# Kernel tuning notes

Hardware: AMD Instinct MI355X
Metric: run time of the kernel (lower is better)

The kernel has to match this reference:

```python
import jax, jax.numpy as jnp
import numpy as np

K_MASK = -2.3819763e+38
B, T, D = 2, 2048, 2048
N, K, H = 8, 2, 256          # query heads, kv heads, head dim
F = 8192                     # ffn hidden
A = 4                        # num_altup_inputs
P = 4                        # num_modalities
WINDOW = 512
SOFT_CAP = 50.0
Q_SCALE = H ** -0.5
ROPE_BASE = 10000.0


def rms_norm(x, scale=None, eps=1e-6):
    y = x * jax.lax.rsqrt(jnp.mean(jnp.square(x), axis=-1, keepdims=True) + eps)
    if scale is not None:
        y = y * (1.0 + scale)   # scale_plus_one=True
    return y


def apply_rope(x, pos, base=ROPE_BASE, scale_factor=1.0):
    # x: [B,T,num_heads,H], pos: [B,T]
    h = x.shape[-1]
    frac = 2.0 * jnp.arange(h // 2, dtype=jnp.float32) / h
    timescale = base ** frac
    sin_inp = (pos[..., None].astype(jnp.float32) / timescale)[..., None, :] / scale_factor  # [B,T,1,H/2]
    sin, cos = jnp.sin(sin_inp), jnp.cos(sin_inp)
    x1, x2 = jnp.split(x, 2, axis=-1)
    return jnp.concatenate([x1 * cos - x2 * sin, x2 * cos + x1 * sin], axis=-1).astype(x.dtype)


def setup_inputs():
    key = jax.random.key(0)
    ks = jax.random.split(key, 12)
    r = lambda i, shape, s=0.02: jax.random.normal(ks[i], shape, dtype=jnp.float32) * s
    pos = jnp.broadcast_to(jnp.arange(T, dtype=jnp.int32), (B, T))
    causal = pos[:, :, None] >= pos[:, None, :]  # [B,T,T] bool
    return dict(
        x=jax.random.normal(ks[0], (A, B, T, D), dtype=jnp.float32),
        segment_pos=pos,
        attn_mask=causal,
        router_w=r(1, (D, P), 1.0),
        pred_coefs=r(2, (P, A, A), 0.0001),
        corr_coefs=r(3, (P, A), 0.01),
        correct_output_scale=jnp.ones((D,), jnp.float32),
        pre_attn_scale=jnp.zeros((D,), jnp.float32),
        q_w=r(4, (N, D, H)),
        kv_w=r(5, (2, K, D, H)),
        qk_q_scale=jnp.zeros((H,), jnp.float32),
        qk_k_scale=jnp.zeros((H,), jnp.float32),
        o_w=r(6, (N, H, D)),
        post_attn_scale=jnp.zeros((D,), jnp.float32),
        pre_ffw_scale=jnp.zeros((D,), jnp.float32),
        gate_w=r(7, (D, F)),
        up_w=r(8, (D, F)),
        down_w=r(9, (F, D)),
        post_ffw_scale=jnp.zeros((D,), jnp.float32),
    )


def _router(h, router_w):
    # modality router: scale by 1/d_model, project, tanh in fp32
    return jnp.tanh(jnp.einsum('btd,dp->btp', h * (1.0 / D), router_w).astype(jnp.float32))


def _attention(x, segment_pos, attn_mask, q_w, kv_w, qk_q_scale, qk_k_scale, o_w):
    q = jnp.einsum('btd,ndh->btnh', x, q_w)               # [B,T,N,H]
    k, v = jnp.einsum('bsd,ckdh->cbskh', x, kv_w)         # each [B,T,K,H]
    q = rms_norm(q, qk_q_scale)                           # qk norm
    k = rms_norm(k, qk_k_scale)
    v = rms_norm(v)                                       # value norm (no scale)
    q = apply_rope(q, segment_pos) * Q_SCALE
    k = apply_rope(k, segment_pos)
    g = N // K                                            # GQA group size
    qr = q.reshape(B, T, K, g, H)
    logits = jnp.einsum('btkgh,bskh->btkgs', qr, k).reshape(B, T, N, T)
    logits = jnp.tanh(logits / SOFT_CAP) * SOFT_CAP       # attn_logits_soft_cap
    # sliding-window mask combined with causal attn_mask
    sliding = (segment_pos[:, None, :] > segment_pos[:, :, None] - WINDOW) & \
              (segment_pos[:, None, :] < segment_pos[:, :, None] + WINDOW)
    mask = attn_mask & sliding
    padded = jnp.where(mask[:, :, None, :], logits, K_MASK)
    probs = jax.nn.softmax(padded, axis=-1).astype(k.dtype)
    enc = jnp.einsum('btkgs,bskh->btkgh', probs.reshape(B, T, K, g, T), v).reshape(B, T, N, H)
    return jnp.einsum('btnh,nhd->btd', enc, o_w)


def reference(x, segment_pos, attn_mask, router_w, pred_coefs, corr_coefs,
              correct_output_scale, pre_attn_scale, q_w, kv_w, qk_q_scale, qk_k_scale,
              o_w, post_attn_scale, pre_ffw_scale, gate_w, up_w, down_w, post_ffw_scale):
    # ---- AltUp predict ----
    mods = _router(x[0], router_w)                                   # [B,T,P]
    coefs = jnp.einsum('btp,pij->btij', mods, pred_coefs.astype(jnp.float32))
    predictions = x + jnp.einsum('btij,jbtd->ibtd', coefs, x).astype(x.dtype)
    active = predictions[0]
    # ---- attention block ----
    attn_in = rms_norm(active, pre_attn_scale)
    attn = _attention(attn_in, segment_pos, attn_mask, q_w, kv_w, qk_q_scale, qk_k_scale, o_w)
    attn = rms_norm(attn, post_attn_scale)
    attn_gated = active + attn
    # ---- gated-GELU MLP ----
    h = rms_norm(attn_gated, pre_ffw_scale)
    ffw = jnp.einsum('btf,fd->btd', jax.nn.gelu(h @ gate_w) * (h @ up_w), down_w)
    ffw = rms_norm(ffw, post_ffw_scale)
    activated = attn_gated + ffw
    # ---- AltUp correct (with scale_corrected_output) ----
    activated = activated * correct_output_scale
    mods_c = _router(activated, router_w)
    c = jnp.einsum('btp,pi->bti', mods_c, corr_coefs.astype(jnp.float32)) + 1.0
    innovation = activated - predictions[0]
    corrected = predictions + jnp.einsum('bti,btd->ibtd', c, innovation).astype(x.dtype)
    return corrected
```

## Files before the change

### kernel.cpp

```cpp
#include <hip/hip_runtime.h>
#include <hip/hip_bf16.h>

typedef unsigned short u16;
typedef __attribute__((ext_vector_type(8))) short bf16x8_t;
typedef __attribute__((ext_vector_type(4))) float f32x4_t;

#define DEV __device__ __forceinline__

constexpr int cB = 2, cT = 2048, cD = 2048;
constexpr int cN = 8, cK = 2, cH = 256, cF = 8192;
constexpr int cBT = cB * cT;
constexpr float cEPS = 1e-6f;
constexpr float cQS = 0.0625f;
constexpr float cCAP = 50.0f;
constexpr int cWIN = 512;
constexpr int cNH = 12;

DEV u16 f2bf(float f) {
  union { float f; unsigned u; } c; c.f = f;
  unsigned u = c.u;
  return (u16)((u + 0x7fffu + ((u >> 16) & 1u)) >> 16);
}
DEV float bf2f(u16 h) {
  union { unsigned u; float f; } c; c.u = ((unsigned)h) << 16;
  return c.f;
}
DEV float g4(const float4& v, int k) { return k == 0 ? v.x : k == 1 ? v.y : k == 2 ? v.z : v.w; }
DEV void store_bf4(u16* p, float a, float b, float c, float d) {
  union { u16 h[4]; uint2 v; } o;
  o.h[0] = f2bf(a); o.h[1] = f2bf(b); o.h[2] = f2bf(c); o.h[3] = f2bf(d);
  *(uint2*)p = o.v;
}
DEV float tanh_fast(float x) {
  float e2 = __expf(2.0f * x);
  return 1.0f - 2.0f * __builtin_amdgcn_rcpf(e2 + 1.0f);
}
DEV float gelu_fast(float x) {
  float u = 1.5957691216057308f * (x + 0.044715f * x * x * x);
  float e2 = __expf(u);
  return x * (1.0f - __builtin_amdgcn_rcpf(e2 + 1.0f));
}

DEV float block_sum256(float v, float* sbuf) {
  #pragma unroll
  for (int m = 32; m > 0; m >>= 1) v += __shfl_xor(v, m, 64);
  int wid = threadIdx.x >> 6;
  if ((threadIdx.x & 63) == 0) sbuf[wid] = v;
  __syncthreads();
  float tot = sbuf[0] + sbuf[1] + sbuf[2] + sbuf[3];
  __syncthreads();
  return tot;
}
DEV void block_sum256x4(float v[4], float* sbuf ) {
  #pragma unroll
  for (int m = 32; m > 0; m >>= 1) {
    #pragma unroll
    for (int k = 0; k < 4; k++) v[k] += __shfl_xor(v[k], m, 64);
  }
  int wid = threadIdx.x >> 6;
  if ((threadIdx.x & 63) == 0) *(float4*)(sbuf + wid * 4) = make_float4(v[0], v[1], v[2], v[3]);
  __syncthreads();
  #pragma unroll
  for (int k = 0; k < 4; k++) v[k] = sbuf[k] + sbuf[4 + k] + sbuf[8 + k] + sbuf[12 + k];
  __syncthreads();
}

#define GLD_LDS16(gp, lp) __builtin_amdgcn_global_load_lds( \
    (const __attribute__((address_space(1))) void*)(gp),    \
    (__attribute__((address_space(3))) void*)(lp), 16, 0, 0)

#define WAITV(n) asm volatile("s_waitcnt vmcnt(" #n ")" ::: "memory")
#define LGKM(n)  asm volatile("s_waitcnt lgkmcnt(" #n ")" ::: "memory")
#define SCHED0() __builtin_amdgcn_sched_barrier(0)
#define LDS_ADDR(p) ((unsigned)(uintptr_t)(__attribute__((address_space(3))) const void*)(p))
#define DSR(dst, base, off) \
  asm volatile("ds_read_b128 %0, %1 offset:" off : "=v"(dst) : "v"(base))

__global__ __launch_bounds__(256) void k_transpose_cast(
    const float* __restrict__ src, u16* __restrict__ dst, int R, int C, int gu) {
  __shared__ float tile[64][65];
  size_t base = (size_t)blockIdx.z * R * C;
  int c0 = blockIdx.x * 64, r0 = blockIdx.y * 64;
  int tx = threadIdx.x & 15, ty = threadIdx.x >> 4;
  #pragma unroll
  for (int i = 0; i < 4; i++) {
    int r = ty + i * 16;
    float4 v = *(const float4*)(src + base + (size_t)(r0 + r) * C + c0 + tx * 4);
    tile[r][tx * 4 + 0] = v.x; tile[r][tx * 4 + 1] = v.y;
    tile[r][tx * 4 + 2] = v.z; tile[r][tx * 4 + 3] = v.w;
  }
  __syncthreads();
  #pragma unroll
  for (int i = 0; i < 4; i++) {
    int j = ty + i * 16;
    int c = c0 + j;
    int n = (gu < 0) ? c : (((c >> 4) << 5) + (gu << 4) + (c & 15));
    store_bf4(dst + base + (size_t)n * R + r0 + tx * 4,
              tile[tx * 4 + 0][j], tile[tx * 4 + 1][j],
              tile[tx * 4 + 2][j], tile[tx * 4 + 3][j]);
  }
}

__global__ __launch_bounds__(256) void k_rope_table(
    const int* __restrict__ pos, float2* __restrict__ rt) {
  int idx = blockIdx.x * 256 + threadIdx.x;
  int bt = idx >> 7, j = idx & 127;
  float p = (float)pos[bt];
  float ts = powf(10000.0f, (2.0f * j) * (1.0f / cH));
  float si = p / ts;
  rt[idx] = make_float2(sinf(si), cosf(si));
}

__global__ __launch_bounds__(256) void k_predict(
    const float* __restrict__ x, const float* __restrict__ router_w,
    const float* __restrict__ pred_coefs, const float* __restrict__ pre_attn_scale,
    float* __restrict__ out, u16* __restrict__ attn_in) {
  __shared__ float sbuf[16];
  int bt = blockIdx.x, tid = threadIdx.x;
  const size_t PL = (size_t)cBT * cD;
  const size_t rowb = (size_t)bt * cD;
  float4 xv[4][2];
  #pragma unroll
  for (int j = 0; j < 4; j++)
    #pragma unroll
    for (int u = 0; u < 2; u++)
      xv[j][u] = *(const float4*)(x + j * PL + rowb + (u * 256 + tid) * 4);
  float rp[4] = {0, 0, 0, 0};
  #pragma unroll
  for (int u = 0; u < 2; u++)
    #pragma unroll
    for (int k = 0; k < 4; k++) {
      int e = (u * 256 + tid) * 4 + k;
      float4 rw = *(const float4*)(router_w + (size_t)e * 4);
      float xe = g4(xv[0][u], k);
      rp[0] += xe * rw.x; rp[1] += xe * rw.y; rp[2] += xe * rw.z; rp[3] += xe * rw.w;
    }
  block_sum256x4(rp, sbuf);
  float mods[4];
  #pragma unroll
  for (int p = 0; p < 4; p++) mods[p] = tanh_fast(rp[p] * (1.0f / cD));
  float coef[4][4];
  #pragma unroll
  for (int i = 0; i < 4; i++)
    #pragma unroll
    for (int j = 0; j < 4; j++) {
      float s = 0;
      #pragma unroll
      for (int p = 0; p < 4; p++) s += mods[p] * pred_coefs[(p * 4 + i) * 4 + j];
      coef[i][j] = s;
    }
  float4 p04[2]; float ssq = 0;
  #pragma unroll
  for (int u = 0; u < 2; u++)
    #pragma unroll
    for (int i = 0; i < 4; i++) {
      float4 s = xv[i][u];
      #pragma unroll
      for (int j = 0; j < 4; j++) {
        s.x += coef[i][j] * xv[j][u].x; s.y += coef[i][j] * xv[j][u].y;
        s.z += coef[i][j] * xv[j][u].z; s.w += coef[i][j] * xv[j][u].w;
      }
      *(float4*)(out + i * PL + rowb + (u * 256 + tid) * 4) = s;
      if (i == 0) { p04[u] = s; ssq += s.x * s.x + s.y * s.y + s.z * s.z + s.w * s.w; }
    }
  float rs = rsqrtf(block_sum256(ssq, sbuf) * (1.0f / cD) + cEPS);
  #pragma unroll
  for (int u = 0; u < 2; u++) {
    int e0 = (u * 256 + tid) * 4;
    float4 sc = *(const float4*)(pre_attn_scale + e0);
    store_bf4(attn_in + rowb + e0,
              p04[u].x * rs * (1.0f + sc.x), p04[u].y * rs * (1.0f + sc.y),
              p04[u].z * rs * (1.0f + sc.z), p04[u].w * rs * (1.0f + sc.w));
  }
}

template <int OUT_MODE>
__global__ __launch_bounds__(512, 2) void k_gemm8p(
    const u16* __restrict__ A, const u16* __restrict__ Bt, void* __restrict__ Cv,
    int Nn, int Kk) {
  constexpr int MI = 8;
  constexpr int A_KS = 256 * 32;
  constexpr int B_KS = 256 * 32;
  constexpr int BUF_E = 2 * A_KS + 2 * B_KS;
  extern __shared__ u16 lds[];

  const int tid = threadIdx.x;
  const int wid = tid >> 6, lane = tid & 63;
  const int wr = wid >> 2, wc = wid & 3;
  const int fr = lane & 15, fq = lane >> 4;

  const int nwg = gridDim.x * gridDim.y;
  const int flat = blockIdx.y * gridDim.x + blockIdx.x;
  const int swz = (flat & 7) * (nwg >> 3) + (flat >> 3);
  const int m0 = (swz % gridDim.x) * 256;
  const int n0 = (swz / gridDim.x) * 256;
  const int NT = Kk >> 6;
  const int NH = NT * 2;

  const int srow = lane >> 2, sslot = lane & 3;
  const int scol = (sslot ^ ((srow >> 1) & 3)) * 8;
  const u16* aSrc0 = A + (size_t)(m0 + wid * 16 + srow) * Kk + scol;
  const u16* aSrc1 = A + (size_t)(m0 + 128 + wid * 16 + srow) * Kk + scol;
  const u16* bSrc0 = Bt + (size_t)(n0 + wid * 16 + srow) * Kk + scol;
  const u16* bSrc1 = Bt + (size_t)(n0 + 128 + wid * 16 + srow) * Kk + scol;

  const int swzR = (fq ^ ((fr >> 1) & 3)) * 8;
  const unsigned base0 = LDS_ADDR(lds);
  const unsigned aoffB = (unsigned)(((wr * 128 + fr) * 32 + swzR) * 2);
  const unsigned boffB = (unsigned)((2 * A_KS + (wc * 64 + fr) * 32 + swzR) * 2);
  const unsigned aB0 = base0 + aoffB, aB1 = base0 + BUF_E * 2 + aoffB;
  const unsigned bB0 = base0 + boffB, bB1 = base0 + BUF_E * 2 + boffB;

  auto stageH = [&](int h) {
    int tt = h >> 1, ks = h & 1;
    int koff = h * 32;
    u16* dstA = lds + (tt & 1) * BUF_E + ks * A_KS + wid * 512;
    GLD_LDS16(aSrc0 + koff, dstA);
    GLD_LDS16(aSrc1 + koff, dstA + 128 * 32);
    u16* dstB = lds + (tt & 1) * BUF_E + 2 * A_KS + ks * B_KS + wid * 512;
    GLD_LDS16(bSrc0 + koff, dstB);
    GLD_LDS16(bSrc1 + koff, dstB + 128 * 32);
  };

  f32x4_t acc[MI][4];
  #pragma unroll
  for (int i = 0; i < MI; i++)
    #pragma unroll
    for (int j = 0; j < 4; j++) acc[i][j] = (f32x4_t){0.f, 0.f, 0.f, 0.f};

  bf16x8_t aX[8], aY[8], bX[4], bY[4];

#define READS_KS0(ab, bb, av, bv) do {                                   \
    DSR(av[0], ab, "0");     DSR(av[1], ab, "1024");                     \
    DSR(av[2], ab, "2048");  DSR(av[3], ab, "3072");                     \
    DSR(av[4], ab, "4096");  DSR(av[5], ab, "5120");                     \
    DSR(av[6], ab, "6144");  DSR(av[7], ab, "7168");                     \
    DSR(bv[0], bb, "0");     DSR(bv[1], bb, "1024");                     \
    DSR(bv[2], bb, "2048");  DSR(bv[3], bb, "3072");  } while (0)
#define READS_KS1(ab, bb, av, bv) do {                                   \
    DSR(av[0], ab, "16384"); DSR(av[1], ab, "17408");                    \
    DSR(av[2], ab, "18432"); DSR(av[3], ab, "19456");                    \
    DSR(av[4], ab, "20480"); DSR(av[5], ab, "21504");                    \
    DSR(av[6], ab, "22528"); DSR(av[7], ab, "23552");                    \
    DSR(bv[0], bb, "16384"); DSR(bv[1], bb, "17408");                    \
    DSR(bv[2], bb, "18432"); DSR(bv[3], bb, "19456"); } while (0)

#define MFMA32(av, bv)                                                    \
  __builtin_amdgcn_s_setprio(1);                                          \
  _Pragma("unroll")                                                       \
  for (int i = 0; i < 8; i++) {                                           \
    acc[i][0] = __builtin_amdgcn_mfma_f32_16x16x32_bf16(av[i], bv[0], acc[i][0], 0, 0, 0); \
    acc[i][1] = __builtin_amdgcn_mfma_f32_16x16x32_bf16(av[i], bv[1], acc[i][1], 0, 0, 0); \
    acc[i][2] = __builtin_amdgcn_mfma_f32_16x16x32_bf16(av[i], bv[2], acc[i][2], 0, 0, 0); \
    acc[i][3] = __builtin_amdgcn_mfma_f32_16x16x32_bf16(av[i], bv[3], acc[i][3], 0, 0, 0); \
  }                                                                       \
  __builtin_amdgcn_s_setprio(0);

  stageH(0); asm volatile("" ::: "memory");
  stageH(1); asm volatile("" ::: "memory");
  stageH(2);
  WAITV(8);
  __builtin_amdgcn_s_barrier();
  SCHED0();
  READS_KS0(aB0, bB0, aX, bX);

  for (int t = 0; t < NT; t++) {
    const unsigned aPb = (t & 1) ? aB1 : aB0;
    const unsigned bPb = (t & 1) ? bB1 : bB0;
    const unsigned aNb = (t & 1) ? aB0 : aB1;
    const unsigned bNb = (t & 1) ? bB0 : bB1;

    {
      const int R = NH - 1 - 2 * t;
      if (R >= 2) WAITV(4); else WAITV(0);
      __builtin_amdgcn_s_barrier();
      SCHED0();
      if (R >= 3) stageH(2 * t + 3);
      READS_KS1(aPb, bPb, aY, bY);
      LGKM(12);
      SCHED0();
      MFMA32(aX, bX)
    }
    {
      const int R = NH - 2 - 2 * t;
      if (R >= 2) WAITV(4); else if (R == 1) WAITV(0);
      __builtin_amdgcn_s_barrier();
      SCHED0();
      if (R >= 3) stageH(2 * t + 4);
      if (R >= 1) {
        READS_KS0(aNb, bNb, aX, bX);
        LGKM(12);
      } else {
        LGKM(0);
      }
      SCHED0();
      MFMA32(aY, bY)
    }
  }
#undef MFMA32
#undef READS_KS0
#undef READS_KS1

  if constexpr (OUT_MODE == 2) {
    const int Nh = Nn >> 1;
    #pragma unroll
    for (int i = 0; i < MI; i++)
      #pragma unroll
      for (int jp = 0; jp < 2; jp++) {
        int c = (n0 + wc * 64 + jp * 32) / 2 + fr;
        #pragma unroll
        for (int r = 0; r < 4; r++) {
          int m = m0 + wr * (MI * 16) + i * 16 + fq * 4 + r;
          float g = acc[i][2 * jp][r], uu = acc[i][2 * jp + 1][r];
          ((u16*)Cv)[(size_t)m * Nh + c] = f2bf(gelu_fast(g) * uu);
        }
      }
  } else {
    #pragma unroll
    for (int i = 0; i < MI; i++)
      #pragma unroll
      for (int j = 0; j < 4; j++)
        #pragma unroll
        for (int r = 0; r < 4; r++) {
          int m = m0 + wr * (MI * 16) + i * 16 + fq * 4 + r;
          int n = n0 + wc * 64 + j * 16 + fr;
          ((u16*)Cv)[(size_t)m * Nn + n] = f2bf(acc[i][j][r]);
        }
  }
}

template <int OUT_MODE>
__global__ __launch_bounds__(512, 2) void k_gemm4p(
    const u16* __restrict__ A, const u16* __restrict__ Bt, void* __restrict__ Cv,
    int Nn, int Kk) {
  constexpr int A_KS = 128 * 32;
  constexpr int B_KS = 256 * 32;
  constexpr int SLOT_E = 2 * A_KS + 2 * B_KS;
  constexpr unsigned SLOT_B = 49152;
  extern __shared__ u16 lds[];

  const int tid = threadIdx.x;
  const int wid = tid >> 6, lane = tid & 63;
  const int wr = wid >> 2, wc = wid & 3;
  const int fr = lane & 15, fq = lane >> 4;

  const int nwg = gridDim.x * gridDim.y;
  const int flat = blockIdx.y * gridDim.x + blockIdx.x;
  const int swz = (flat & 7) * (nwg >> 3) + (flat >> 3);
  const int m0 = (swz % gridDim.x) * 128;
  const int n0 = (swz / gridDim.x) * 256;
  const int NT = Kk >> 6;
  const int NH = NT * 2;

  const int srow = lane >> 2, sslot = lane & 3;
  const int scol = (sslot ^ ((srow >> 1) & 3)) * 8;
  const u16* aSrc  = A + (size_t)(m0 + wid * 16 + srow) * Kk + scol;
  const u16* bSrc0 = Bt + (size_t)(n0 + wid * 16 + srow) * Kk + scol;
  const u16* bSrc1 = Bt + (size_t)(n0 + 128 + wid * 16 + srow) * Kk + scol;

  const int swzR = (fq ^ ((fr >> 1) & 3)) * 8;
  const unsigned base0 = LDS_ADDR(lds);
  const unsigned aoffB = (unsigned)(((wr * 64 + fr) * 32 + swzR) * 2);
  const unsigned boffB = (unsigned)((2 * A_KS + (wc * 64 + fr) * 32 + swzR) * 2);
  const unsigned aS0 = base0 + aoffB;
  const unsigned bS0 = base0 + boffB;
  const unsigned aLast = aS0 + 2 * SLOT_B, bLast = bS0 + 2 * SLOT_B;

  unsigned aCur = aS0, bCur = bS0;
  unsigned aNxt = aS0 + SLOT_B, bNxt = bS0 + SLOT_B;

  auto stageH = [&](int h) {
    int tt = h >> 1, ks = h & 1;
    int slot = tt % 3;
    int koff = h * 32;
    u16* dstA = lds + slot * SLOT_E + ks * A_KS + wid * 512;
    GLD_LDS16(aSrc + koff, dstA);
    u16* dstB = lds + slot * SLOT_E + 2 * A_KS + ks * B_KS + wid * 512;
    GLD_LDS16(bSrc0 + koff, dstB);
    GLD_LDS16(bSrc1 + koff, dstB + 128 * 32);
  };

  f32x4_t acc[4][4];
  #pragma unroll
  for (int i = 0; i < 4; i++)
    #pragma unroll
    for (int j = 0; j < 4; j++) acc[i][j] = (f32x4_t){0.f, 0.f, 0.f, 0.f};

  bf16x8_t aX[4], aY[4], bX[4], bY[4];

#define R4_KS0(ab, bb, av, bv) do {                                      \
    DSR(av[0], ab, "0");     DSR(av[1], ab, "1024");                     \
    DSR(av[2], ab, "2048");  DSR(av[3], ab, "3072");                     \
    DSR(bv[0], bb, "0");     DSR(bv[1], bb, "1024");                     \
    DSR(bv[2], bb, "2048");  DSR(bv[3], bb, "3072");  } while (0)
#define R4_KS1(ab, bb, av, bv) do {                                      \
    DSR(av[0], ab, "8192");  DSR(av[1], ab, "9216");                     \
    DSR(av[2], ab, "10240"); DSR(av[3], ab, "11264");                    \
    DSR(bv[0], bb, "16384"); DSR(bv[1], bb, "17408");                    \
    DSR(bv[2], bb, "18432"); DSR(bv[3], bb, "19456"); } while (0)

#define MFMA16(av, bv)                                                    \
  __builtin_amdgcn_s_setprio(1);                                          \
  _Pragma("unroll")                                                       \
  for (int i = 0; i < 4; i++) {                                           \
    acc[i][0] = __builtin_amdgcn_mfma_f32_16x16x32_bf16(av[i], bv[0], acc[i][0], 0, 0, 0); \
    acc[i][1] = __builtin_amdgcn_mfma_f32_16x16x32_bf16(av[i], bv[1], acc[i][1], 0, 0, 0); \
    acc[i][2] = __builtin_amdgcn_mfma_f32_16x16x32_bf16(av[i], bv[2], acc[i][2], 0, 0, 0); \
    acc[i][3] = __builtin_amdgcn_mfma_f32_16x16x32_bf16(av[i], bv[3], acc[i][3], 0, 0, 0); \
  }                                                                       \
  __builtin_amdgcn_s_setprio(0);

  stageH(0); asm volatile("" ::: "memory");
  stageH(1); asm volatile("" ::: "memory");
  stageH(2); asm volatile("" ::: "memory");
  stageH(3);
  WAITV(9);
  __builtin_amdgcn_s_barrier();
  SCHED0();
  R4_KS0(aCur, bCur, aX, bX);

  for (int t = 0; t < NT; t++) {
    {
      const int R = NH - 1 - 2 * t;
      if (R >= 3) WAITV(6); else WAITV(0);
      __builtin_amdgcn_s_barrier();
      SCHED0();
      if (R >= 4) stageH(2 * t + 4);
      R4_KS1(aCur, bCur, aY, bY);
      LGKM(8);
      SCHED0();
      MFMA16(aX, bX)
    }
    {
      const int R = NH - 2 - 2 * t;
      if (R >= 3) WAITV(6); else if (R == 2) WAITV(3); else if (R == 1) WAITV(0);
      __builtin_amdgcn_s_barrier();
      SCHED0();
      if (R >= 4) stageH(2 * t + 5);
      if (R >= 1) {
        R4_KS0(aNxt, bNxt, aX, bX);
        LGKM(8);
      } else {
        LGKM(0);
      }
      SCHED0();
      MFMA16(aY, bY)
    }
    aCur = aNxt; bCur = bNxt;
    aNxt = (aNxt == aLast) ? aS0 : aNxt + SLOT_B;
    bNxt = (bNxt == bLast) ? bS0 : bNxt + SLOT_B;
  }
#undef MFMA16
#undef R4_KS0
#undef R4_KS1

  #pragma unroll
  for (int i = 0; i < 4; i++)
    #pragma unroll
    for (int j = 0; j < 4; j++)
      #pragma unroll
      for (int r = 0; r < 4; r++) {
        int m = m0 + wr * 64 + i * 16 + fq * 4 + r;
        int n = n0 + wc * 64 + j * 16 + fr;
        float v = acc[i][j][r];
        if (OUT_MODE == 1) ((u16*)Cv)[(size_t)m * Nn + n] = f2bf(v);
        else ((float*)Cv)[(size_t)m * Nn + n] = v;
      }
}

__global__ __launch_bounds__(64) void k_qkvpost(
    u16* __restrict__ qkv, const float* __restrict__ qscale,
    const float* __restrict__ kscale, const float2* __restrict__ rt,
    u16* __restrict__ vT) {
  int h = blockIdx.x % cNH, bt = blockIdx.x / cNH;
  int lane = threadIdx.x;
  u16* row = qkv + ((size_t)bt * cNH + h) * cH;
  float v[4], ssq = 0;
  #pragma unroll
  for (int m = 0; m < 4; m++) { v[m] = bf2f(row[lane + 64 * m]); ssq += v[m] * v[m]; }
  #pragma unroll
  for (int mm = 32; mm > 0; mm >>= 1) ssq += __shfl_xor(ssq, mm, 64);
  float rs = rsqrtf(ssq * (1.0f / cH) + cEPS);
  if (h < 10) {
    const float* sc = (h < 8) ? qscale : kscale;
    float os = (h < 8) ? cQS : 1.0f;
    #pragma unroll
    for (int m = 0; m < 4; m++) {
      int e = lane + 64 * m;
      v[m] = v[m] * rs * (1.0f + sc[e]);
    }
    #pragma unroll
    for (int m = 0; m < 2; m++) {
      int j = lane + 64 * m;
      float2 t = rt[bt * 128 + j];
      float x1 = v[m], x2 = v[m + 2];
      row[j]       = f2bf((x1 * t.y - x2 * t.x) * os);
      row[j + 128] = f2bf((x2 * t.y + x1 * t.x) * os);
    }
  } else {
    int kk = h - 10;
    int b = bt / cT, t = bt % cT;
    #pragma unroll
    for (int m = 0; m < 4; m++) {
      int e = lane + 64 * m;
      vT[((size_t)(b * cK + kk) * cH + e) * cT + t] = f2bf(v[m] * rs);
    }
  }
}

__global__ __launch_bounds__(128) void k_attn(
    const u16* __restrict__ qkv, const u16* __restrict__ vT, u16* __restrict__ enc) {
  int t0 = blockIdx.x * 16;
  int n = blockIdx.y, b = blockIdx.z;
  int kn = n >> 2;
  int w = threadIdx.x >> 6;
  int lane = threadIdx.x & 63;
  int fr = lane & 15, fq = lane >> 4;
  __shared__ float smem[64 * 69];
  float* P = smem + w * 528;

  bf16x8_t qf[8];
  const u16* qrow = qkv + ((size_t)(b * cT + t0 + fr) * cNH + n) * cH;
  #pragma unroll
  for (int ks = 0; ks < 8; ks++) qf[ks] = *(const bf16x8_t*)(qrow + ks * 32 + fq * 8);

  f32x4_t acc[16];
  #pragma unroll
  for (int ht = 0; ht < 16; ht++) acc[ht] = (f32x4_t){0.f, 0.f, 0.f, 0.f};
  float psum[4] = {0.f, 0.f, 0.f, 0.f};

  int s_lo = t0 - (cWIN - 1); if (s_lo < 0) s_lo = 0; s_lo &= ~31;
  for (int s0 = s_lo + 32 * w; s0 <= t0 + 15; s0 += 64) {
    f32x4_t S[2];
    S[0] = (f32x4_t){0.f, 0.f, 0.f, 0.f};
    S[1] = (f32x4_t){0.f, 0.f, 0.f, 0.f};
    #pragma unroll
    for (int c = 0; c < 2; c++) {
      const u16* krow = qkv + ((size_t)(b * cT + s0 + c * 16 + fr) * cNH + 8 + kn) * cH;
      #pragma unroll
      for (int ks = 0; ks < 8; ks++) {
        bf16x8_t kf = *(const bf16x8_t*)(krow + ks * 32 + fq * 8);
        S[c] = __builtin_amdgcn_mfma_f32_16x16x32_bf16(qf[ks], kf, S[c], 0, 0, 0);
      }
    }
    #pragma unroll
    for (int c = 0; c < 2; c++) {
      int s = s0 + c * 16 + fr;
      #pragma unroll
      for (int r = 0; r < 4; r++) {
        int t = t0 + fq * 4 + r;
        float l = cCAP * tanh_fast(S[c][r] * (1.0f / cCAP));
        float pe = (s <= t && s >= t - (cWIN - 1)) ? __expf(l) : 0.0f;
        psum[r] += pe;
        P[(fq * 4 + r) * 33 + c * 16 + fr] = pe;
      }
    }
    bf16x8_t pf;
    #pragma unroll
    for (int e = 0; e < 8; e++) pf[e] = (short)f2bf(P[fr * 33 + fq * 8 + e]);
    #pragma unroll
    for (int ht = 0; ht < 16; ht++) {
      bf16x8_t vf = *(const bf16x8_t*)(vT + (((size_t)(b * cK + kn)) * cH + ht * 16 + fr) * cT + s0 + fq * 8);
      acc[ht] = __builtin_amdgcn_mfma_f32_16x16x32_bf16(pf, vf, acc[ht], 0, 0, 0);
    }
  }

  __syncthreads();
  if (w == 1) {
    float* row = smem + lane * 69;
    #pragma unroll
    for (int ht = 0; ht < 16; ht++)
      #pragma unroll
      for (int r = 0; r < 4; r++) row[ht * 4 + r] = acc[ht][r];
    #pragma unroll
    for (int r = 0; r < 4; r++) row[64 + r] = psum[r];
  }
  __syncthreads();
  if (w == 0) {
    const float* row = smem + lane * 69;
    #pragma unroll
    for (int ht = 0; ht < 16; ht++)
      #pragma unroll
      for (int r = 0; r < 4; r++) acc[ht][r] += row[ht * 4 + r];
    #pragma unroll
    for (int r = 0; r < 4; r++) psum[r] += row[64 + r];
    #pragma unroll
    for (int r = 0; r < 4; r++) {
      #pragma unroll
      for (int m = 1; m < 16; m <<= 1) psum[r] += __shfl_xor(psum[r], m, 64);
    }
    float inv[4];
    #pragma unroll
    for (int r = 0; r < 4; r++) inv[r] = 1.0f / psum[r];
    #pragma unroll
    for (int ht = 0; ht < 16; ht++)
      #pragma unroll
      for (int r = 0; r < 4; r++)
        enc[(((size_t)(b * cT + t0 + fq * 4 + r)) * cN + n) * cH + ht * 16 + fr] =
            f2bf(acc[ht][r] * inv[r]);
  }
}

__global__ __launch_bounds__(256) void k_postattn(
    const float* __restrict__ attn_raw, const float* __restrict__ out0,
    const float* __restrict__ post_attn_scale, const float* __restrict__ pre_ffw_scale,
    float* __restrict__ ag, u16* __restrict__ h) {
  __shared__ float sbuf[4];
  int bt = blockIdx.x, tid = threadIdx.x;
  const size_t rowb = (size_t)bt * cD;
  float4 ar[2]; float ssq = 0;
  #pragma unroll
  for (int u = 0; u < 2; u++) {
    ar[u] = *(const float4*)(attn_raw + rowb + (u * 256 + tid) * 4);
    ssq += ar[u].x * ar[u].x + ar[u].y * ar[u].y + ar[u].z * ar[u].z + ar[u].w * ar[u].w;
  }
  float rs = rsqrtf(block_sum256(ssq, sbuf) * (1.0f / cD) + cEPS);
  float4 agv[2]; float ssq2 = 0;
  #pragma unroll
  for (int u = 0; u < 2; u++) {
    int e0 = (u * 256 + tid) * 4;
    float4 o0 = *(const float4*)(out0 + rowb + e0);
    float4 sc = *(const float4*)(post_attn_scale + e0);
    float4 a;
    a.x = o0.x + ar[u].x * rs * (1.0f + sc.x);
    a.y = o0.y + ar[u].y * rs * (1.0f + sc.y);
    a.z = o0.z + ar[u].z * rs * (1.0f + sc.z);
    a.w = o0.w + ar[u].w * rs * (1.0f + sc.w);
    agv[u] = a;
    *(float4*)(ag + rowb + e0) = a;
    ssq2 += a.x * a.x + a.y * a.y + a.z * a.z + a.w * a.w;
  }
  float rs2 = rsqrtf(block_sum256(ssq2, sbuf) * (1.0f / cD) + cEPS);
  #pragma unroll
  for (int u = 0; u < 2; u++) {
    int e0 = (u * 256 + tid) * 4;
    float4 sc = *(const float4*)(pre_ffw_scale + e0);
    store_bf4(h + rowb + e0,
              agv[u].x * rs2 * (1.0f + sc.x), agv[u].y * rs2 * (1.0f + sc.y),
              agv[u].z * rs2 * (1.0f + sc.z), agv[u].w * rs2 * (1.0f + sc.w));
  }
}

__global__ __launch_bounds__(256) void k_final(
    const float* __restrict__ ffw_raw, const float* __restrict__ ag,
    const float* __restrict__ post_ffw_scale, const float* __restrict__ cos_scale,
    const float* __restrict__ router_w, const float* __restrict__ corr_coefs,
    float* __restrict__ out) {
  __shared__ float sbuf[16];
  int bt = blockIdx.x, tid = threadIdx.x;
  const size_t PL = (size_t)cBT * cD;
  const size_t rowb = (size_t)bt * cD;
  float4 fv[2]; float ssq = 0;
  #pragma unroll
  for (int u = 0; u < 2; u++) {
    fv[u] = *(const float4*)(ffw_raw + rowb + (u * 256 + tid) * 4);
    ssq += fv[u].x * fv[u].x + fv[u].y * fv[u].y + fv[u].z * fv[u].z + fv[u].w * fv[u].w;
  }
  float rs = rsqrtf(block_sum256(ssq, sbuf) * (1.0f / cD) + cEPS);
  float4 av[2];
  float rp[4] = {0, 0, 0, 0};
  #pragma unroll
  for (int u = 0; u < 2; u++) {
    int e0 = (u * 256 + tid) * 4;
    float4 agx = *(const float4*)(ag + rowb + e0);
    float4 ps = *(const float4*)(post_ffw_scale + e0);
    float4 cs = *(const float4*)(cos_scale + e0);
    float4 a;
    a.x = (agx.x + fv[u].x * rs * (1.0f + ps.x)) * cs.x;
    a.y = (agx.y + fv[u].y * rs * (1.0f + ps.y)) * cs.y;
    a.z = (agx.z + fv[u].z * rs * (1.0f + ps.z)) * cs.z;
    a.w = (agx.w + fv[u].w * rs * (1.0f + ps.w)) * cs.w;
    av[u] = a;
    #pragma unroll
    for (int k = 0; k < 4; k++) {
      float4 rw = *(const float4*)(router_w + (size_t)(e0 + k) * 4);
      float xe = g4(a, k);
      rp[0] += xe * rw.x; rp[1] += xe * rw.y; rp[2] += xe * rw.z; rp[3] += xe * rw.w;
    }
  }
  block_sum256x4(rp, sbuf);
  float cc[4];
  #pragma unroll
  for (int i = 0; i < 4; i++) {
    float s = 1.0f;
    #pragma unroll
    for (int p = 0; p < 4; p++) s += tanh_fast(rp[p] * (1.0f / cD)) * corr_coefs[p * 4 + i];
    cc[i] = s;
  }
  #pragma unroll
  for (int u = 0; u < 2; u++) {
    size_t o = rowb + (u * 256 + tid) * 4;
    float4 p0 = *(const float4*)(out + o);
    float4 in4;
    in4.x = av[u].x - p0.x; in4.y = av[u].y - p0.y;
    in4.z = av[u].z - p0.z; in4.w = av[u].w - p0.w;
    float4 w0;
    w0.x = p0.x + cc[0] * in4.x; w0.y = p0.y + cc[0] * in4.y;
    w0.z = p0.z + cc[0] * in4.z; w0.w = p0.w + cc[0] * in4.w;
    *(float4*)(out + o) = w0;
    #pragma unroll
    for (int i = 1; i < 4; i++) {
      float4 q = *(const float4*)(out + i * PL + o);
      q.x += cc[i] * in4.x; q.y += cc[i] * in4.y;
      q.z += cc[i] * in4.z; q.w += cc[i] * in4.w;
      *(float4*)(out + i * PL + o) = q;
    }
  }
}

extern "C" void kernel_launch(void* const* d_in, const int* in_sizes, int n_in,
                              void* d_out, int out_size, void* d_ws, size_t ws_size,
                              hipStream_t stream) {
  const float* x              = (const float*)d_in[0];
  const int*   pos            = (const int*)d_in[1];
  const float* router_w       = (const float*)d_in[3];
  const float* pred_coefs     = (const float*)d_in[4];
  const float* corr_coefs     = (const float*)d_in[5];
  const float* cos_scale      = (const float*)d_in[6];
  const float* pre_attn_scale = (const float*)d_in[7];
  const float* q_w            = (const float*)d_in[8];
  const float* kv_w           = (const float*)d_in[9];
  const float* qk_q_scale     = (const float*)d_in[10];
  const float* qk_k_scale     = (const float*)d_in[11];
  const float* o_w            = (const float*)d_in[12];
  const float* post_attn_scale= (const float*)d_in[13];
  const float* pre_ffw_scale  = (const float*)d_in[14];
  const float* gate_w         = (const float*)d_in[15];
  const float* up_w           = (const float*)d_in[16];
  const float* down_w         = (const float*)d_in[17];
  const float* post_ffw_scale = (const float*)d_in[18];
  float* out = (float*)d_out;

  char* wsp = (char*)d_ws;
  size_t off = 0;
  auto take = [&](size_t nbytes) -> char* {
    char* p = wsp + off;
    off += (nbytes + 255) & ~((size_t)255);
    return p;
  };
  u16* gu_wT    = (u16*)take((size_t)2 * cF * cD * 2);
  u16* down_wT  = (u16*)take((size_t)cD * cF * 2);
  u16* qkv_wT   = (u16*)take((size_t)cNH * cH * cD * 2);
  u16* o_wT     = (u16*)take((size_t)cD * cN * cH * 2);
  u16* attn_in  = (u16*)take((size_t)cBT * cD * 2);
  u16* qkvbuf   = (u16*)take((size_t)cBT * cNH * cH * 2);
  u16* vTbuf    = (u16*)take((size_t)cB * cK * cH * cT * 2);
  u16* encbuf   = (u16*)take((size_t)cBT * cN * cH * 2);
  float* attn_raw = (float*)take((size_t)cBT * cD * 4);
  float* agbuf    = (float*)take((size_t)cBT * cD * 4);
  u16* hbuf     = (u16*)take((size_t)cBT * cD * 2);
  u16* Gcbuf    = (u16*)take((size_t)cBT * cF * 2);
  float* ffw_raw = (float*)take((size_t)cBT * cD * 4);
  float2* ropetab = (float2*)take((size_t)cBT * 128 * 8);
  (void)in_sizes; (void)n_in; (void)out_size; (void)ws_size;

  dim3 blk256(256), blk64(64), blk128(128), blk512(512);
  constexpr unsigned LDS8  = 2 * (2 * 256 * 32 + 2 * 256 * 32) * 2;
  constexpr unsigned LDS4R = 3 * (2 * 128 * 32 + 2 * 256 * 32) * 2;

  k_transpose_cast<<<dim3(cF / 64, cD / 64, 1), blk256, 0, stream>>>(gate_w, gu_wT, cD, cF, 0);
  k_transpose_cast<<<dim3(cF / 64, cD / 64, 1), blk256, 0, stream>>>(up_w, gu_wT, cD, cF, 1);
  k_transpose_cast<<<dim3(cD / 64, cF / 64, 1), blk256, 0, stream>>>(down_w, down_wT, cF, cD, -1);
  k_transpose_cast<<<dim3(cH / 64, cD / 64, cN), blk256, 0, stream>>>(q_w, qkv_wT, cD, cH, -1);
  k_transpose_cast<<<dim3(cH / 64, cD / 64, 2 * cK), blk256, 0, stream>>>(
      kv_w, qkv_wT + (size_t)cN * cH * cD, cD, cH, -1);
  k_transpose_cast<<<dim3(cD / 64, (cN * cH) / 64, 1), blk256, 0, stream>>>(o_w, o_wT, cN * cH, cD, -1);
  k_rope_table<<<dim3(cBT * 128 / 256), blk256, 0, stream>>>(pos, ropetab);

  k_predict<<<dim3(cBT), blk256, 0, stream>>>(x, router_w, pred_coefs, pre_attn_scale, out, attn_in);

  k_gemm4p<1><<<dim3(cBT / 128, (cNH * cH) / 256), blk512, LDS4R, stream>>>(
      attn_in, qkv_wT, qkvbuf, cNH * cH, cD);

  k_qkvpost<<<dim3(cBT * cNH), blk64, 0, stream>>>(qkvbuf, qk_q_scale, qk_k_scale, ropetab, vTbuf);

  k_attn<<<dim3(cT / 16, cN, cB), blk128, 0, stream>>>(qkvbuf, vTbuf, encbuf);

  k_gemm4p<0><<<dim3(cBT / 128, cD / 256), blk512, LDS4R, stream>>>(
      encbuf, o_wT, attn_raw, cD, cN * cH);
  k_postattn<<<dim3(cBT), blk256, 0, stream>>>(attn_raw, out, post_attn_scale, pre_ffw_scale, agbuf, hbuf);

  k_gemm8p<2><<<dim3(cBT / 256, (2 * cF) / 256), blk512, LDS8, stream>>>(
      hbuf, gu_wT, Gcbuf, 2 * cF, cD);
  k_gemm4p<0><<<dim3(cBT / 128, cD / 256), blk512, LDS4R, stream>>>(
      Gcbuf, down_wT, ffw_raw, cD, cF);

  k_final<<<dim3(cBT), blk256, 0, stream>>>(ffw_raw, agbuf, post_ffw_scale, cos_scale,
                                            router_w, corr_coefs, out);
}
```

Before: 933.5 us.

## Recompute AltUp predictions from coefficients and store GEMM outputs in bf16

k_predict no longer writes the four full fp32 prediction planes. It stores only the per-token 4x4 coefficient matrix, and k_postattn and k_final recompute the predictions from x. Separately, the o-proj and down-proj GEMMs now write bf16 instead of fp32 (mode 1), and the downstream kernels read those outputs through a bf16 loader. The aim is to cut global memory traffic in the elementwise kernels, in exchange for re-reading x and a loss of precision in the raw attention and FFW outputs before their RMS norms.

```diff
diff --git a/kernel.cpp b/kernel.cpp
--- a/kernel.cpp
+++ b/kernel.cpp
@@ -31,6 +31,10 @@
   o.h[0] = f2bf(a); o.h[1] = f2bf(b); o.h[2] = f2bf(c); o.h[3] = f2bf(d);
   *(uint2*)p = o.v;
 }
+DEV float4 load_bf4(const u16* p) {
+  union { uint2 v; u16 h[4]; } c; c.v = *(const uint2*)p;
+  return make_float4(bf2f(c.h[0]), bf2f(c.h[1]), bf2f(c.h[2]), bf2f(c.h[3]));
+}
 DEV float tanh_fast(float x) {
   float e2 = __expf(2.0f * x);
   return 1.0f - 2.0f * __builtin_amdgcn_rcpf(e2 + 1.0f);
@@ -114,7 +118,7 @@
 __global__ __launch_bounds__(256) void k_predict(
     const float* __restrict__ x, const float* __restrict__ router_w,
     const float* __restrict__ pred_coefs, const float* __restrict__ pre_attn_scale,
-    float* __restrict__ out, u16* __restrict__ attn_in) {
+    float* __restrict__ coefbuf, u16* __restrict__ attn_in) {
   __shared__ float sbuf[16];
   int bt = blockIdx.x, tid = threadIdx.x;
   const size_t PL = (size_t)cBT * cD;
@@ -149,20 +153,23 @@
       for (int p = 0; p < 4; p++) s += mods[p] * pred_coefs[(p * 4 + i) * 4 + j];
       coef[i][j] = s;
     }
+  if (tid == 0) {
+    #pragma unroll
+    for (int i = 0; i < 4; i++)
+      *(float4*)(coefbuf + (size_t)bt * 16 + i * 4) =
+          make_float4(coef[i][0], coef[i][1], coef[i][2], coef[i][3]);
+  }
   float4 p04[2]; float ssq = 0;
   #pragma unroll
-  for (int u = 0; u < 2; u++)
-    #pragma unroll
-    for (int i = 0; i < 4; i++) {
-      float4 s = xv[i][u];
-      #pragma unroll
-      for (int j = 0; j < 4; j++) {
-        s.x += coef[i][j] * xv[j][u].x; s.y += coef[i][j] * xv[j][u].y;
-        s.z += coef[i][j] * xv[j][u].z; s.w += coef[i][j] * xv[j][u].w;
-      }
-      *(float4*)(out + i * PL + rowb + (u * 256 + tid) * 4) = s;
-      if (i == 0) { p04[u] = s; ssq += s.x * s.x + s.y * s.y + s.z * s.z + s.w * s.w; }
-    }
+  for (int u = 0; u < 2; u++) {
+    float4 s = xv[0][u];
+    #pragma unroll
+    for (int j = 0; j < 4; j++) {
+      s.x += coef[0][j] * xv[j][u].x; s.y += coef[0][j] * xv[j][u].y;
+      s.z += coef[0][j] * xv[j][u].z; s.w += coef[0][j] * xv[j][u].w;
+    }
+    p04[u] = s; ssq += s.x * s.x + s.y * s.y + s.z * s.z + s.w * s.w;
+  }
   float rs = rsqrtf(block_sum256(ssq, sbuf) * (1.0f / cD) + cEPS);
   #pragma unroll
   for (int u = 0; u < 2; u++) {
@@ -602,16 +609,23 @@
 }
 
 __global__ __launch_bounds__(256) void k_postattn(
-    const float* __restrict__ attn_raw, const float* __restrict__ out0,
+    const u16* __restrict__ attn_raw, const float* __restrict__ out0_unused,
     const float* __restrict__ post_attn_scale, const float* __restrict__ pre_ffw_scale,
+    const float* __restrict__ x, const float* __restrict__ coefbuf,
     float* __restrict__ ag, u16* __restrict__ h) {
   __shared__ float sbuf[4];
   int bt = blockIdx.x, tid = threadIdx.x;
+  const size_t PL = (size_t)cBT * cD;
   const size_t rowb = (size_t)bt * cD;
+  float cf0[4];
+  {
+    float4 c0 = *(const float4*)(coefbuf + (size_t)bt * 16);
+    cf0[0] = c0.x; cf0[1] = c0.y; cf0[2] = c0.z; cf0[3] = c0.w;
+  }
   float4 ar[2]; float ssq = 0;
   #pragma unroll
   for (int u = 0; u < 2; u++) {
-    ar[u] = *(const float4*)(attn_raw + rowb + (u * 256 + tid) * 4);
+    ar[u] = load_bf4(attn_raw + rowb + (u * 256 + tid) * 4);
     ssq += ar[u].x * ar[u].x + ar[u].y * ar[u].y + ar[u].z * ar[u].z + ar[u].w * ar[u].w;
   }
   float rs = rsqrtf(block_sum256(ssq, sbuf) * (1.0f / cD) + cEPS);
@@ -619,13 +633,19 @@
   #pragma unroll
   for (int u = 0; u < 2; u++) {
     int e0 = (u * 256 + tid) * 4;
-    float4 o0 = *(const float4*)(out0 + rowb + e0);
+    float4 p0 = *(const float4*)(x + rowb + e0);
+    #pragma unroll
+    for (int j = 0; j < 4; j++) {
+      float4 xj = *(const float4*)(x + j * PL + rowb + e0);
+      p0.x += cf0[j] * xj.x; p0.y += cf0[j] * xj.y;
+      p0.z += cf0[j] * xj.z; p0.w += cf0[j] * xj.w;
+    }
     float4 sc = *(const float4*)(post_attn_scale + e0);
     float4 a;
-    a.x = o0.x + ar[u].x * rs * (1.0f + sc.x);
-    a.y = o0.y + ar[u].y * rs * (1.0f + sc.y);
-    a.z = o0.z + ar[u].z * rs * (1.0f + sc.z);
-    a.w = o0.w + ar[u].w * rs * (1.0f + sc.w);
+    a.x = p0.x + ar[u].x * rs * (1.0f + sc.x);
+    a.y = p0.y + ar[u].y * rs * (1.0f + sc.y);
+    a.z = p0.z + ar[u].z * rs * (1.0f + sc.z);
+    a.w = p0.w + ar[u].w * rs * (1.0f + sc.w);
     agv[u] = a;
     *(float4*)(ag + rowb + e0) = a;
     ssq2 += a.x * a.x + a.y * a.y + a.z * a.z + a.w * a.w;
@@ -642,9 +662,10 @@
 }
 
 __global__ __launch_bounds__(256) void k_final(
-    const float* __restrict__ ffw_raw, const float* __restrict__ ag,
+    const u16* __restrict__ ffw_raw, const float* __restrict__ ag,
     const float* __restrict__ post_ffw_scale, const float* __restrict__ cos_scale,
     const float* __restrict__ router_w, const float* __restrict__ corr_coefs,
+    const float* __restrict__ x, const float* __restrict__ coefbuf,
     float* __restrict__ out) {
   __shared__ float sbuf[16];
   int bt = blockIdx.x, tid = threadIdx.x;
@@ -653,7 +674,7 @@
   float4 fv[2]; float ssq = 0;
   #pragma unroll
   for (int u = 0; u < 2; u++) {
-    fv[u] = *(const float4*)(ffw_raw + rowb + (u * 256 + tid) * 4);
+    fv[u] = load_bf4(ffw_raw + rowb + (u * 256 + tid) * 4);
     ssq += fv[u].x * fv[u].x + fv[u].y * fv[u].y + fv[u].z * fv[u].z + fv[u].w * fv[u].w;
   }
   float rs = rsqrtf(block_sum256(ssq, sbuf) * (1.0f / cD) + cEPS);
@@ -687,23 +708,38 @@
     for (int p = 0; p < 4; p++) s += tanh_fast(rp[p] * (1.0f / cD)) * corr_coefs[p * 4 + i];
     cc[i] = s;
   }
+  float cf[4][4];
+  #pragma unroll
+  for (int i = 0; i < 4; i++) {
+    float4 ci = *(const float4*)(coefbuf + (size_t)bt * 16 + i * 4);
+    cf[i][0] = ci.x; cf[i][1] = ci.y; cf[i][2] = ci.z; cf[i][3] = ci.w;
+  }
   #pragma unroll
   for (int u = 0; u < 2; u++) {
-    size_t o = rowb + (u * 256 + tid) * 4;
-    float4 p0 = *(const float4*)(out + o);
+    int e0 = (u * 256 + tid) * 4;
+    float4 xv[4];
+    #pragma unroll
+    for (int j = 0; j < 4; j++) xv[j] = *(const float4*)(x + j * PL + rowb + e0);
+    float4 pred[4];
+    #pragma unroll
+    for (int i = 0; i < 4; i++) {
+      float4 s = xv[i];
+      #pragma unroll
+      for (int j = 0; j < 4; j++) {
+        s.x += cf[i][j] * xv[j].x; s.y += cf[i][j] * xv[j].y;
+        s.z += cf[i][j] * xv[j].z; s.w += cf[i][j] * xv[j].w;
+      }
+      pred[i] = s;
+    }
     float4 in4;
-    in4.x = av[u].x - p0.x; in4.y = av[u].y - p0.y;
-    in4.z = av[u].z - p0.z; in4.w = av[u].w - p0.w;
-    float4 w0;
-    w0.x = p0.x + cc[0] * in4.x; w0.y = p0.y + cc[0] * in4.y;
-    w0.z = p0.z + cc[0] * in4.z; w0.w = p0.w + cc[0] * in4.w;
-    *(float4*)(out + o) = w0;
-    #pragma unroll
-    for (int i = 1; i < 4; i++) {
-      float4 q = *(const float4*)(out + i * PL + o);
-      q.x += cc[i] * in4.x; q.y += cc[i] * in4.y;
-      q.z += cc[i] * in4.z; q.w += cc[i] * in4.w;
-      *(float4*)(out + i * PL + o) = q;
+    in4.x = av[u].x - pred[0].x; in4.y = av[u].y - pred[0].y;
+    in4.z = av[u].z - pred[0].z; in4.w = av[u].w - pred[0].w;
+    #pragma unroll
+    for (int i = 0; i < 4; i++) {
+      float4 q;
+      q.x = pred[i].x + cc[i] * in4.x; q.y = pred[i].y + cc[i] * in4.y;
+      q.z = pred[i].z + cc[i] * in4.z; q.w = pred[i].w + cc[i] * in4.w;
+      *(float4*)(out + i * PL + rowb + e0) = q;
     }
   }
 }
@@ -746,12 +782,13 @@
   u16* qkvbuf   = (u16*)take((size_t)cBT * cNH * cH * 2);
   u16* vTbuf    = (u16*)take((size_t)cB * cK * cH * cT * 2);
   u16* encbuf   = (u16*)take((size_t)cBT * cN * cH * 2);
-  float* attn_raw = (float*)take((size_t)cBT * cD * 4);
+  u16* attn_raw = (u16*)take((size_t)cBT * cD * 2);
   float* agbuf    = (float*)take((size_t)cBT * cD * 4);
   u16* hbuf     = (u16*)take((size_t)cBT * cD * 2);
   u16* Gcbuf    = (u16*)take((size_t)cBT * cF * 2);
-  float* ffw_raw = (float*)take((size_t)cBT * cD * 4);
+  u16* ffw_raw  = (u16*)take((size_t)cBT * cD * 2);
   float2* ropetab = (float2*)take((size_t)cBT * 128 * 8);
+  float* coefbuf  = (float*)take((size_t)cBT * 16 * 4);
   (void)in_sizes; (void)n_in; (void)out_size; (void)ws_size;
 
   dim3 blk256(256), blk64(64), blk128(128), blk512(512);
@@ -767,7 +804,8 @@
   k_transpose_cast<<<dim3(cD / 64, (cN * cH) / 64, 1), blk256, 0, stream>>>(o_w, o_wT, cN * cH, cD, -1);
   k_rope_table<<<dim3(cBT * 128 / 256), blk256, 0, stream>>>(pos, ropetab);
 
-  k_predict<<<dim3(cBT), blk256, 0, stream>>>(x, router_w, pred_coefs, pre_attn_scale, out, attn_in);
+  k_predict<<<dim3(cBT), blk256, 0, stream>>>(x, router_w, pred_coefs, pre_attn_scale,
+                                              coefbuf, attn_in);
 
   k_gemm4p<1><<<dim3(cBT / 128, (cNH * cH) / 256), blk512, LDS4R, stream>>>(
       attn_in, qkv_wT, qkvbuf, cNH * cH, cD);
@@ -776,15 +814,16 @@
 
   k_attn<<<dim3(cT / 16, cN, cB), blk128, 0, stream>>>(qkvbuf, vTbuf, encbuf);
 
-  k_gemm4p<0><<<dim3(cBT / 128, cD / 256), blk512, LDS4R, stream>>>(
+  k_gemm4p<1><<<dim3(cBT / 128, cD / 256), blk512, LDS4R, stream>>>(
       encbuf, o_wT, attn_raw, cD, cN * cH);
-  k_postattn<<<dim3(cBT), blk256, 0, stream>>>(attn_raw, out, post_attn_scale, pre_ffw_scale, agbuf, hbuf);
+  k_postattn<<<dim3(cBT), blk256, 0, stream>>>(attn_raw, nullptr, post_attn_scale,
+                                               pre_ffw_scale, x, coefbuf, agbuf, hbuf);
 
   k_gemm8p<2><<<dim3(cBT / 256, (2 * cF) / 256), blk512, LDS8, stream>>>(
       hbuf, gu_wT, Gcbuf, 2 * cF, cD);
-  k_gemm4p<0><<<dim3(cBT / 128, cD / 256), blk512, LDS4R, stream>>>(
+  k_gemm4p<1><<<dim3(cBT / 128, cD / 256), blk512, LDS4R, stream>>>(
       Gcbuf, down_wT, ffw_raw, cD, cF);
 
   k_final<<<dim3(cBT), blk256, 0, stream>>>(ffw_raw, agbuf, post_ffw_scale, cos_scale,
-                                            router_w, corr_coefs, out);
-}
+                                            router_w, corr_coefs, x, coefbuf, out);
+}
```

Result: faster. 890.6 us (-4.6%).
